# Kernel optimization log

Measured on AMD Instinct MI355X. Metric: run time of the kernel, lower is better.

## Reference

```python
import jax, jax.numpy as jnp
import numpy as np
import math

B, S, D, H = 4, 2048, 512, 8
DK = D // H


def setup_inputs() -> dict:
    key = jax.random.key(0)
    ks = jax.random.split(key, 12)
    def lin(k, scale):
        return jax.random.normal(k, (D, D), dtype=jnp.float32) * scale
    s = 1.0 / math.sqrt(D)
    return {
        "q": jax.random.normal(ks[0], (B, S, D), dtype=jnp.float32),
        "k": jax.random.normal(ks[1], (B, S, D), dtype=jnp.float32),
        "v": jax.random.normal(ks[2], (B, S, D), dtype=jnp.float32),
        "mask": jax.random.randint(ks[3], (B, S, S), 0, 2, dtype=jnp.int32),
        "Wq": lin(ks[4], s), "bq": jnp.zeros((D,), jnp.float32),
        "Wk": lin(ks[5], s), "bk": jnp.zeros((D,), jnp.float32),
        "Wv": lin(ks[6], s), "bv": jnp.zeros((D,), jnp.float32),
        "Wo": lin(ks[7], s), "bo": jnp.zeros((D,), jnp.float32),
    }


def reference(q, k, v, mask, Wq, bq, Wk, bk, Wv, bv, Wo, bo):
    bs = q.shape[0]
    # torch Linear: y = x @ W.T + b
    qh = (q @ Wq.T + bq).reshape(bs, -1, H, DK).transpose(0, 2, 1, 3)  # [b,h,s,dk]
    kh = (k @ Wk.T + bk).reshape(bs, -1, H, DK).transpose(0, 2, 1, 3)
    vh = (v @ Wv.T + bv).reshape(bs, -1, H, DK).transpose(0, 2, 1, 3)
    scores = jnp.einsum("bhqd,bhkd->bhqk", qh, kh) / math.sqrt(DK)
    scores = jnp.where(mask[:, None, :, :] == 0, jnp.float32(-1e9), scores)
    scores = jax.nn.softmax(scores, axis=-1)
    # dropout p=0.0 -> identity
    concat = jnp.einsum("bhqk,bhkd->bhqd", scores, vh)
    concat = concat.transpose(0, 2, 1, 3).reshape(bs, -1, D)
    output = concat @ Wo.T + bo
    return (output, scores)
```

## Files before the change

### kernel.cpp

```cpp
#include <hip/hip_runtime.h>
#include <hip/hip_bf16.h>

#define B_ 4
#define S_ 2048
#define D_ 512
#define H_ 8
#define DK_ 64
#define M_ (B_*S_)

typedef float f32x4 __attribute__((ext_vector_type(4)));
typedef __bf16 bf16x8 __attribute__((ext_vector_type(8)));
typedef unsigned short u16x8 __attribute__((ext_vector_type(8)));

static __device__ __forceinline__ unsigned short f2bf(float x) {
    return __builtin_bit_cast(unsigned short, __float2bfloat16(x));
}
static __device__ __forceinline__ float bf2f(unsigned short u) {
    return __bfloat162float(__builtin_bit_cast(__hip_bfloat16, u));
}
static __device__ __forceinline__ bf16x8 ldfrag(const unsigned short* p) {
    return __builtin_bit_cast(bf16x8, *(const u16x8*)p);
}

static __device__ __forceinline__ void bar_lds() {
    asm volatile("s_waitcnt lgkmcnt(0)\n\ts_barrier" ::: "memory");
}

typedef __attribute__((address_space(1))) const unsigned int gu32;
typedef __attribute__((address_space(3))) unsigned int lu32;
static __device__ __forceinline__ void gl_lds16(const unsigned short* g, unsigned short* l) {
    __builtin_amdgcn_global_load_lds((gu32*)g, (lu32*)l, 16, 0, 0);
}

static __device__ __forceinline__ void split8(const float4 x0, const float4 x1,
                                              u16x8& h, u16x8& l) {
    float f[8] = {x0.x, x0.y, x0.z, x0.w, x1.x, x1.y, x1.z, x1.w};
    #pragma unroll
    for (int j = 0; j < 8; ++j) {
        const unsigned u = __builtin_bit_cast(unsigned, f[j]);
        h[j] = (unsigned short)(u >> 16);
        const float hf = __builtin_bit_cast(float, u & 0xFFFF0000u);
        l[j] = (unsigned short)(__builtin_bit_cast(unsigned, f[j] - hf) >> 16);
    }
}

__global__ __launch_bounds__(256) void split_x3(
    const float* __restrict__ xq, const float* __restrict__ xk, const float* __restrict__ xv,
    unsigned short* __restrict__ qh, unsigned short* __restrict__ qlo,
    unsigned short* __restrict__ kh, unsigned short* __restrict__ klo,
    unsigned short* __restrict__ vh, unsigned short* __restrict__ vlo)
{
    const size_t t = (size_t)blockIdx.x * 256 + threadIdx.x;
    const int z = blockIdx.y;
    const float* in = z == 0 ? xq : z == 1 ? xk : xv;
    unsigned short* oh = z == 0 ? qh : z == 1 ? kh : vh;
    unsigned short* ol = z == 0 ? qlo : z == 1 ? klo : vlo;
    const float4* p = (const float4*)(in + t * 8);
    u16x8 hh, ll;
    split8(p[0], p[1], hh, ll);
    ((u16x8*)oh)[t] = hh;
    ((u16x8*)ol)[t] = ll;
}

__global__ __launch_bounds__(256) void split_w4(
    const float* __restrict__ Wq, const float* __restrict__ Wk,
    const float* __restrict__ Wv, const float* __restrict__ Wo,
    unsigned short* __restrict__ Wcat_h, unsigned short* __restrict__ Wcat_l,
    unsigned short* __restrict__ Wo_h, unsigned short* __restrict__ Wo_l)
{
    const size_t t = (size_t)blockIdx.x * 256 + threadIdx.x;
    const int z = blockIdx.y;
    const float* in = z == 0 ? Wq : z == 1 ? Wk : z == 2 ? Wv : Wo;
    unsigned short* oh = z < 3 ? Wcat_h + (size_t)z * 262144 : Wo_h;
    unsigned short* ol = z < 3 ? Wcat_l + (size_t)z * 262144 : Wo_l;
    const float4* p = (const float4*)(in + t * 8);
    u16x8 hh, ll;
    split8(p[0], p[1], hh, ll);
    ((u16x8*)oh)[t] = hh;
    ((u16x8*)ol)[t] = ll;
}

__global__ __launch_bounds__(256) void mask_pack(
    const int* __restrict__ mask, unsigned long long* __restrict__ bits)
{
    const size_t t = (size_t)blockIdx.x * 256 + threadIdx.x;
    const int m = mask[t];
    const unsigned long long w = __ballot(m != 0);
    if ((threadIdx.x & 63) == 0) bits[t >> 6] = w;
}

#define GBK 32
__global__ __launch_bounds__(256, 2) void gemm_hl(
    const unsigned short* __restrict__ qXh, const unsigned short* __restrict__ qXl,
    const unsigned short* __restrict__ kXh, const unsigned short* __restrict__ kXl,
    const unsigned short* __restrict__ vXh, const unsigned short* __restrict__ vXl,
    const unsigned short* __restrict__ Wh, const unsigned short* __restrict__ Wl,
    const float* __restrict__ b0, const float* __restrict__ b1, const float* __restrict__ b2,
    float* __restrict__ Yf32,
    unsigned short* __restrict__ q_hi, unsigned short* __restrict__ q_lo,
    unsigned short* __restrict__ k_hi, unsigned short* __restrict__ k_lo,
    unsigned short* __restrict__ v_hi, int fused)
{
    __shared__ __align__(16) unsigned short lds[2][4][128 * GBK];

    const int tid = threadIdx.x;
    const int lane = tid & 63, wv = tid >> 6;
    const int quad = lane >> 4, col = lane & 15;
    const int wm = wv >> 1, wn = wv & 1;
    const int m0 = blockIdx.x * 128;
    const int n0g = blockIdx.y * 128;
    const int mat = fused ? (n0g >> 9) : 0;
    const unsigned short* Xh = (!fused || mat == 0) ? qXh : (mat == 1 ? kXh : vXh);
    const unsigned short* Xl = (!fused || mat == 0) ? qXl : (mat == 1 ? kXl : vXl);

    const int rsub = lane >> 2;
    const int csw = (((lane & 3) ^ ((lane >> 3) & 3))) * 8;

    f32x4 acc[4][4] = {};

    auto STAGE = [&](int t, int buf) {
        const int kt = t * GBK;
        #pragma unroll
        for (int i = 0; i < 2; ++i) {
            const int r0 = wv * 32 + i * 16;
            gl_lds16(Xh + (size_t)(m0 + r0 + rsub) * D_ + kt + csw, &lds[buf][0][r0 * GBK]);
            gl_lds16(Xl + (size_t)(m0 + r0 + rsub) * D_ + kt + csw, &lds[buf][1][r0 * GBK]);
            gl_lds16(Wh + (size_t)(n0g + r0 + rsub) * D_ + kt + csw, &lds[buf][2][r0 * GBK]);
            gl_lds16(Wl + (size_t)(n0g + r0 + rsub) * D_ + kt + csw, &lds[buf][3][r0 * GBK]);
        }
    };

    auto COMPUTE = [&](int buf) {
        bf16x8 ah[4], al[4], bh[4], bl[4];
        #pragma unroll
        for (int i = 0; i < 4; ++i) {
            const int ra = wm * 64 + i * 16 + col;
            const int ca = (quad ^ ((ra >> 1) & 3)) * 8;
            ah[i] = ldfrag(&lds[buf][0][ra * GBK + ca]);
            al[i] = ldfrag(&lds[buf][1][ra * GBK + ca]);
            const int rb = wn * 64 + i * 16 + col;
            const int cb = (quad ^ ((rb >> 1) & 3)) * 8;
            bh[i] = ldfrag(&lds[buf][2][rb * GBK + cb]);
            bl[i] = ldfrag(&lds[buf][3][rb * GBK + cb]);
        }
        __builtin_amdgcn_s_setprio(1);
        #pragma unroll
        for (int i = 0; i < 4; ++i)
            #pragma unroll
            for (int j = 0; j < 4; ++j) {
                acc[i][j] = __builtin_amdgcn_mfma_f32_16x16x32_bf16(ah[i], bh[j], acc[i][j], 0, 0, 0);
                acc[i][j] = __builtin_amdgcn_mfma_f32_16x16x32_bf16(al[i], bh[j], acc[i][j], 0, 0, 0);
                acc[i][j] = __builtin_amdgcn_mfma_f32_16x16x32_bf16(ah[i], bl[j], acc[i][j], 0, 0, 0);
            }
        __builtin_amdgcn_s_setprio(0);
    };

    STAGE(0, 0);
    STAGE(1, 1);
    int cur = 0;
    for (int t = 0; t < 16; ++t) {
        if (t < 15) asm volatile("s_waitcnt vmcnt(8)\n\ts_barrier" ::: "memory");
        else        asm volatile("s_waitcnt vmcnt(0)\n\ts_barrier" ::: "memory");
        COMPUTE(cur);
        asm volatile("s_barrier" ::: "memory");
        if (t < 14) STAGE(t + 2, cur);
        cur ^= 1;
    }

    #pragma unroll
    for (int j = 0; j < 4; ++j) {
        const int ng = n0g + wn * 64 + j * 16 + col;
        const int n = fused ? (ng & 511) : ng;
        const float bias = fused ? (mat == 0 ? b0[n] : mat == 1 ? b1[n] : b2[n]) : b0[n];
        #pragma unroll
        for (int i = 0; i < 4; ++i) {
            #pragma unroll
            for (int r = 0; r < 4; ++r) {
                const int m = m0 + wm * 64 + i * 16 + quad * 4 + r;
                const float vv = acc[i][j][r] + bias;
                if (!fused) {
                    Yf32[(size_t)m * D_ + n] = vv;
                } else {
                    const int bi = m >> 11, si = m & (S_ - 1);
                    const int hh = n >> 6, dk = n & 63;
                    const size_t idx = (((size_t)bi * H_ + hh) * S_ + si) * DK_ + dk;
                    const unsigned short hi = f2bf(vv);
                    if (mat == 0)      { q_hi[idx] = hi; q_lo[idx] = f2bf(vv - bf2f(hi)); }
                    else if (mat == 1) { k_hi[idx] = hi; k_lo[idx] = f2bf(vv - bf2f(hi)); }
                    else               { v_hi[idx] = hi; }
                }
            }
        }
    }
}

__global__ __launch_bounds__(256) void attn_mfma_kernel(
    const unsigned short* __restrict__ q_hi, const unsigned short* __restrict__ q_lo,
    const unsigned short* __restrict__ k_hi, const unsigned short* __restrict__ k_lo,
    const unsigned short* __restrict__ v_hi, const unsigned long long* __restrict__ mbits,
    float* __restrict__ scores,
    unsigned short* __restrict__ ch, unsigned short* __restrict__ cl)
{
    __shared__ __align__(16) unsigned short sK2[2][64][72];
    __shared__ __align__(16) unsigned short sVt[64][72];
    __shared__ __align__(16) unsigned short sP[64][72];

    const int tid = threadIdx.x;
    const int q0 = blockIdx.x * 64;
    const int h = blockIdx.y, b = blockIdx.z;
    const size_t bh = (size_t)b * H_ + h;
    const int wv = tid >> 6, lane = tid & 63, quad = lane >> 4, col = lane & 15;
    const int sr = tid >> 2, sc = (tid & 3) * 16;

    float* sPF = (float*)&sK2[0][0][0];

    bf16x8 qh[2], ql[2];
    {
        const size_t qb = (bh * S_ + q0 + wv * 16 + col) * DK_;
        qh[0] = ldfrag(q_hi + qb + quad * 8);
        qh[1] = ldfrag(q_hi + qb + 32 + quad * 8);
        ql[0] = ldfrag(q_lo + qb + quad * 8);
        ql[1] = ldfrag(q_lo + qb + 32 + quad * 8);
    }

    const size_t mrow_base = ((size_t)b * S_ + q0 + wv * 16 + quad * 4) * (S_ / 64);

    u16x8 rkh[2], rkl[2], rv[2];
    auto ld_k = [&](int kt) {
        const u16x8* gh = (const u16x8*)(k_hi + (bh * S_ + kt * 64 + sr) * DK_ + sc);
        const u16x8* gl = (const u16x8*)(k_lo + (bh * S_ + kt * 64 + sr) * DK_ + sc);
        rkh[0] = gh[0]; rkh[1] = gh[1]; rkl[0] = gl[0]; rkl[1] = gl[1];
    };
    auto ld_v = [&](int kt) {
        const u16x8* gv = (const u16x8*)(v_hi + (bh * S_ + kt * 64 + sr) * DK_ + sc);
        rv[0] = gv[0]; rv[1] = gv[1];
    };

    auto compute_svals = [&](const unsigned long long* mw, float sv[4][4]) {
        #pragma unroll
        for (int t = 0; t < 4; ++t) {
            f32x4 acc = {0.f, 0.f, 0.f, 0.f};
            __builtin_amdgcn_s_setprio(1);
            #pragma unroll
            for (int kci = 0; kci < 2; ++kci) {
                bf16x8 bhf = ldfrag(&sK2[0][t * 16 + col][kci * 32 + quad * 8]);
                bf16x8 blf = ldfrag(&sK2[1][t * 16 + col][kci * 32 + quad * 8]);
                acc = __builtin_amdgcn_mfma_f32_16x16x32_bf16(qh[kci], bhf, acc, 0, 0, 0);
                acc = __builtin_amdgcn_mfma_f32_16x16x32_bf16(qh[kci], blf, acc, 0, 0, 0);
                acc = __builtin_amdgcn_mfma_f32_16x16x32_bf16(ql[kci], bhf, acc, 0, 0, 0);
            }
            __builtin_amdgcn_s_setprio(0);
            #pragma unroll
            for (int r = 0; r < 4; ++r) {
                float s = acc[r] * 0.125f;
                if (!((mw[r] >> (t * 16 + col)) & 1ull)) s = -1e9f;
                sv[t][r] = s;
            }
        }
    };

    float m_run[4], l_run[4];
    #pragma unroll
    for (int r = 0; r < 4; ++r) { m_run[r] = -1e30f; l_run[r] = 0.f; }

    ld_k(0);
    for (int kt = 0; kt < 32; ++kt) {
        bar_lds();
        *(u16x8*)&sK2[0][sr][sc] = rkh[0]; *(u16x8*)&sK2[0][sr][sc + 8] = rkh[1];
        *(u16x8*)&sK2[1][sr][sc] = rkl[0]; *(u16x8*)&sK2[1][sr][sc + 8] = rkl[1];
        bar_lds();
        if (kt < 31) ld_k(kt + 1);
        unsigned long long mw[4];
        #pragma unroll
        for (int r = 0; r < 4; ++r) mw[r] = mbits[mrow_base + (size_t)r * (S_ / 64) + kt];
        float sv[4][4];
        compute_svals(mw, sv);
        #pragma unroll
        for (int r = 0; r < 4; ++r) {
            float tm = fmaxf(fmaxf(sv[0][r], sv[1][r]), fmaxf(sv[2][r], sv[3][r]));
            #pragma unroll
            for (int mm = 1; mm < 16; mm <<= 1) tm = fmaxf(tm, __shfl_xor(tm, mm));
            const float nm = fmaxf(m_run[r], tm);
            float ts = __expf(sv[0][r] - nm) + __expf(sv[1][r] - nm)
                     + __expf(sv[2][r] - nm) + __expf(sv[3][r] - nm);
            #pragma unroll
            for (int mm = 1; mm < 16; mm <<= 1) ts += __shfl_xor(ts, mm);
            l_run[r] = l_run[r] * __expf(m_run[r] - nm) + ts;
            m_run[r] = nm;
        }
    }
    float inv_l[4];
    #pragma unroll
    for (int r = 0; r < 4; ++r) inv_l[r] = 1.f / l_run[r];

    f32x4 oacc[4] = {};
    ld_k(0); ld_v(0);
    for (int kt = 0; kt < 32; ++kt) {
        bar_lds();
        *(u16x8*)&sK2[0][sr][sc] = rkh[0]; *(u16x8*)&sK2[0][sr][sc + 8] = rkh[1];
        *(u16x8*)&sK2[1][sr][sc] = rkl[0]; *(u16x8*)&sK2[1][sr][sc + 8] = rkl[1];
        #pragma unroll
        for (int i = 0; i < 8; ++i) { sVt[sc + i][sr] = rv[0][i]; sVt[sc + 8 + i][sr] = rv[1][i]; }
        bar_lds();
        if (kt < 31) { ld_k(kt + 1); ld_v(kt + 1); }
        unsigned long long mw[4];
        #pragma unroll
        for (int r = 0; r < 4; ++r) mw[r] = mbits[mrow_base + (size_t)r * (S_ / 64) + kt];
        float sv[4][4];
        compute_svals(mw, sv);
        float pv[4][4];
        #pragma unroll
        for (int t = 0; t < 4; ++t) {
            #pragma unroll
            for (int r = 0; r < 4; ++r) {
                const float p = __expf(sv[t][r] - m_run[r]) * inv_l[r];
                pv[t][r] = p;
                sP[wv * 16 + quad * 4 + r][t * 16 + col] = f2bf(p);
            }
        }
        bar_lds();
        #pragma unroll
        for (int t = 0; t < 4; ++t)
            #pragma unroll
            for (int r = 0; r < 4; ++r)
                sPF[(wv * 16 + quad * 4 + r) * 68 + t * 16 + col] = pv[t][r];
        #pragma unroll
        for (int rg = 0; rg < 2; ++rg)
            #pragma unroll
            for (int hf = 0; hf < 2; ++hf) {
                const int rl = wv * 16 + rg * 8 + (lane >> 3);
                const int cf = hf * 32 + (lane & 7) * 4;
                const f32x4 pw = *(const f32x4*)&sPF[rl * 68 + cf];
                __builtin_nontemporal_store(pw,
                    (f32x4*)&scores[(bh * S_ + q0 + rl) * S_ + kt * 64 + cf]);
            }
        __builtin_amdgcn_s_setprio(1);
        #pragma unroll
        for (int to = 0; to < 4; ++to) {
            #pragma unroll
            for (int kc = 0; kc < 64; kc += 32) {
                bf16x8 a  = ldfrag(&sP[wv * 16 + col][kc + quad * 8]);
                bf16x8 bb = ldfrag(&sVt[to * 16 + col][kc + quad * 8]);
                oacc[to] = __builtin_amdgcn_mfma_f32_16x16x32_bf16(a, bb, oacc[to], 0, 0, 0);
            }
        }
        __builtin_amdgcn_s_setprio(0);
    }

    #pragma unroll
    for (int to = 0; to < 4; ++to) {
        #pragma unroll
        for (int r = 0; r < 4; ++r) {
            const int qg = q0 + wv * 16 + quad * 4 + r;
            const size_t idx = ((size_t)b * S_ + qg) * D_ + h * DK_ + to * 16 + col;
            const float o = oacc[to][r];
            const unsigned short oh16 = f2bf(o);
            ch[idx] = oh16;
            cl[idx] = f2bf(o - bf2f(oh16));
        }
    }
}

extern "C" void kernel_launch(void* const* d_in, const int* in_sizes, int n_in,
                              void* d_out, int out_size, void* d_ws, size_t ws_size,
                              hipStream_t stream) {
    const float* q  = (const float*)d_in[0];
    const float* k  = (const float*)d_in[1];
    const float* v  = (const float*)d_in[2];
    const int* mask = (const int*)d_in[3];
    const float* Wq = (const float*)d_in[4];  const float* bq = (const float*)d_in[5];
    const float* Wk = (const float*)d_in[6];  const float* bk = (const float*)d_in[7];
    const float* Wv = (const float*)d_in[8];  const float* bv = (const float*)d_in[9];
    const float* Wo = (const float*)d_in[10]; const float* bo = (const float*)d_in[11];

    float* out    = (float*)d_out;
    float* scores = out + (size_t)B_ * S_ * D_;

    const size_t NH = (size_t)B_ * H_ * S_ * DK_;
    unsigned short* W = (unsigned short*)d_ws;
    unsigned short* q_hi = W + 0 * NH;
    unsigned short* q_lo = W + 1 * NH;
    unsigned short* k_hi = W + 2 * NH;
    unsigned short* k_lo = W + 3 * NH;
    unsigned short* v_hi = W + 4 * NH;
    unsigned short* qXh = W + 7 * NH;  unsigned short* qXl = W + 8 * NH;
    unsigned short* kXh = W + 9 * NH;  unsigned short* kXl = W + 10 * NH;
    unsigned short* vXh = W + 11 * NH; unsigned short* vXl = W + 12 * NH;
    unsigned short* cat_h = qXh;       unsigned short* cat_l = qXl;
    unsigned short* Wcat_h = W + 13 * NH;
    unsigned short* Wcat_l = Wcat_h + 786432;
    unsigned short* Wo_h   = Wcat_l + 786432;
    unsigned short* Wo_l   = Wo_h + 262144;
    unsigned long long* mbits = (unsigned long long*)(Wo_l + 262144);

    split_x3<<<dim3(2048, 3), 256, 0, stream>>>(q, k, v, qXh, qXl, kXh, kXl, vXh, vXl);
    split_w4<<<dim3(128, 4), 256, 0, stream>>>(Wq, Wk, Wv, Wo, Wcat_h, Wcat_l, Wo_h, Wo_l);
    mask_pack<<<dim3(65536), 256, 0, stream>>>(mask, mbits);

    gemm_hl<<<dim3(64, 12), 256, 0, stream>>>(
        qXh, qXl, kXh, kXl, vXh, vXl, Wcat_h, Wcat_l, bq, bk, bv,
        nullptr, q_hi, q_lo, k_hi, k_lo, v_hi, 1);

    attn_mfma_kernel<<<dim3(S_ / 64, H_, B_), 256, 0, stream>>>(
        q_hi, q_lo, k_hi, k_lo, v_hi, mbits, scores, cat_h, cat_l);

    gemm_hl<<<dim3(64, 4), 256, 0, stream>>>(
        cat_h, cat_l, nullptr, nullptr, nullptr, nullptr, Wo_h, Wo_l, bo, nullptr, nullptr,
        out, nullptr, nullptr, nullptr, nullptr, nullptr, 0);
}
```

Measured before the change: 917.3 us.

## Load K and V fragments directly from global memory, store V transposed

The attention kernel no longer stages K and V tiles through LDS with barriers. Instead each wave loads its MFMA fragments straight from global memory, and V is written pre-transposed by the projection GEMM so the fragments are contiguous. The probability tile also moves to its own LDS array, which drops a barrier. This removes LDS staging and synchronisation, but every wave now re-reads K/V from global or L2 with no register prefetch, and the transposed V store from the GEMM is strided. There is also no barrier between writing sP/sPF and the cross-lane reads, which relies on per-wave row ownership.

```diff
diff --git a/kernel.cpp b/kernel.cpp
--- a/kernel.cpp
+++ b/kernel.cpp
@@ -20,10 +20,6 @@
 }
 static __device__ __forceinline__ bf16x8 ldfrag(const unsigned short* p) {
     return __builtin_bit_cast(bf16x8, *(const u16x8*)p);
-}
-
-static __device__ __forceinline__ void bar_lds() {
-    asm volatile("s_waitcnt lgkmcnt(0)\n\ts_barrier" ::: "memory");
 }
 
 typedef __attribute__((address_space(1))) const unsigned int gu32;
@@ -99,7 +95,7 @@
     float* __restrict__ Yf32,
     unsigned short* __restrict__ q_hi, unsigned short* __restrict__ q_lo,
     unsigned short* __restrict__ k_hi, unsigned short* __restrict__ k_lo,
-    unsigned short* __restrict__ v_hi, int fused)
+    unsigned short* __restrict__ vT, int fused)
 {
     __shared__ __align__(16) unsigned short lds[2][4][128 * GBK];
 
@@ -183,11 +179,15 @@
                 } else {
                     const int bi = m >> 11, si = m & (S_ - 1);
                     const int hh = n >> 6, dk = n & 63;
-                    const size_t idx = (((size_t)bi * H_ + hh) * S_ + si) * DK_ + dk;
                     const unsigned short hi = f2bf(vv);
-                    if (mat == 0)      { q_hi[idx] = hi; q_lo[idx] = f2bf(vv - bf2f(hi)); }
-                    else if (mat == 1) { k_hi[idx] = hi; k_lo[idx] = f2bf(vv - bf2f(hi)); }
-                    else               { v_hi[idx] = hi; }
+                    if (mat == 2) {
+                        const size_t idxT = (((size_t)bi * H_ + hh) * DK_ + dk) * S_ + si;
+                        vT[idxT] = hi;
+                    } else {
+                        const size_t idx = (((size_t)bi * H_ + hh) * S_ + si) * DK_ + dk;
+                        if (mat == 0) { q_hi[idx] = hi; q_lo[idx] = f2bf(vv - bf2f(hi)); }
+                        else          { k_hi[idx] = hi; k_lo[idx] = f2bf(vv - bf2f(hi)); }
+                    }
                 }
             }
         }
@@ -197,22 +197,18 @@
 __global__ __launch_bounds__(256) void attn_mfma_kernel(
     const unsigned short* __restrict__ q_hi, const unsigned short* __restrict__ q_lo,
     const unsigned short* __restrict__ k_hi, const unsigned short* __restrict__ k_lo,
-    const unsigned short* __restrict__ v_hi, const unsigned long long* __restrict__ mbits,
+    const unsigned short* __restrict__ vT, const unsigned long long* __restrict__ mbits,
     float* __restrict__ scores,
     unsigned short* __restrict__ ch, unsigned short* __restrict__ cl)
 {
-    __shared__ __align__(16) unsigned short sK2[2][64][72];
-    __shared__ __align__(16) unsigned short sVt[64][72];
     __shared__ __align__(16) unsigned short sP[64][72];
+    __shared__ __align__(16) float sPF[64][68];
 
     const int tid = threadIdx.x;
     const int q0 = blockIdx.x * 64;
     const int h = blockIdx.y, b = blockIdx.z;
     const size_t bh = (size_t)b * H_ + h;
     const int wv = tid >> 6, lane = tid & 63, quad = lane >> 4, col = lane & 15;
-    const int sr = tid >> 2, sc = (tid & 3) * 16;
-
-    float* sPF = (float*)&sK2[0][0][0];
 
     bf16x8 qh[2], ql[2];
     {
@@ -224,32 +220,25 @@
     }
 
     const size_t mrow_base = ((size_t)b * S_ + q0 + wv * 16 + quad * 4) * (S_ / 64);
-
-    u16x8 rkh[2], rkl[2], rv[2];
-    auto ld_k = [&](int kt) {
-        const u16x8* gh = (const u16x8*)(k_hi + (bh * S_ + kt * 64 + sr) * DK_ + sc);
-        const u16x8* gl = (const u16x8*)(k_lo + (bh * S_ + kt * 64 + sr) * DK_ + sc);
-        rkh[0] = gh[0]; rkh[1] = gh[1]; rkl[0] = gl[0]; rkl[1] = gl[1];
-    };
-    auto ld_v = [&](int kt) {
-        const u16x8* gv = (const u16x8*)(v_hi + (bh * S_ + kt * 64 + sr) * DK_ + sc);
-        rv[0] = gv[0]; rv[1] = gv[1];
-    };
-
-    auto compute_svals = [&](const unsigned long long* mw, float sv[4][4]) {
+    const unsigned short* kH = k_hi + bh * S_ * DK_;
+    const unsigned short* kL = k_lo + bh * S_ * DK_;
+    const unsigned short* vB = vT + bh * DK_ * S_;
+
+    auto compute_svals = [&](int kt, const unsigned long long* mw, float sv[4][4]) {
         #pragma unroll
         for (int t = 0; t < 4; ++t) {
+            const size_t krow = (size_t)(kt * 64 + t * 16 + col) * DK_;
             f32x4 acc = {0.f, 0.f, 0.f, 0.f};
-            __builtin_amdgcn_s_setprio(1);
             #pragma unroll
             for (int kci = 0; kci < 2; ++kci) {
-                bf16x8 bhf = ldfrag(&sK2[0][t * 16 + col][kci * 32 + quad * 8]);
-                bf16x8 blf = ldfrag(&sK2[1][t * 16 + col][kci * 32 + quad * 8]);
+                bf16x8 bhf = ldfrag(kH + krow + kci * 32 + quad * 8);
+                bf16x8 blf = ldfrag(kL + krow + kci * 32 + quad * 8);
+                __builtin_amdgcn_s_setprio(1);
                 acc = __builtin_amdgcn_mfma_f32_16x16x32_bf16(qh[kci], bhf, acc, 0, 0, 0);
                 acc = __builtin_amdgcn_mfma_f32_16x16x32_bf16(qh[kci], blf, acc, 0, 0, 0);
                 acc = __builtin_amdgcn_mfma_f32_16x16x32_bf16(ql[kci], bhf, acc, 0, 0, 0);
-            }
-            __builtin_amdgcn_s_setprio(0);
+                __builtin_amdgcn_s_setprio(0);
+            }
             #pragma unroll
             for (int r = 0; r < 4; ++r) {
                 float s = acc[r] * 0.125f;
@@ -263,18 +252,12 @@
     #pragma unroll
     for (int r = 0; r < 4; ++r) { m_run[r] = -1e30f; l_run[r] = 0.f; }
 
-    ld_k(0);
     for (int kt = 0; kt < 32; ++kt) {
-        bar_lds();
-        *(u16x8*)&sK2[0][sr][sc] = rkh[0]; *(u16x8*)&sK2[0][sr][sc + 8] = rkh[1];
-        *(u16x8*)&sK2[1][sr][sc] = rkl[0]; *(u16x8*)&sK2[1][sr][sc + 8] = rkl[1];
-        bar_lds();
-        if (kt < 31) ld_k(kt + 1);
         unsigned long long mw[4];
         #pragma unroll
         for (int r = 0; r < 4; ++r) mw[r] = mbits[mrow_base + (size_t)r * (S_ / 64) + kt];
         float sv[4][4];
-        compute_svals(mw, sv);
+        compute_svals(kt, mw, sv);
         #pragma unroll
         for (int r = 0; r < 4; ++r) {
             float tm = fmaxf(fmaxf(sv[0][r], sv[1][r]), fmaxf(sv[2][r], sv[3][r]));
@@ -294,57 +277,43 @@
     for (int r = 0; r < 4; ++r) inv_l[r] = 1.f / l_run[r];
 
     f32x4 oacc[4] = {};
-    ld_k(0); ld_v(0);
     for (int kt = 0; kt < 32; ++kt) {
-        bar_lds();
-        *(u16x8*)&sK2[0][sr][sc] = rkh[0]; *(u16x8*)&sK2[0][sr][sc + 8] = rkh[1];
-        *(u16x8*)&sK2[1][sr][sc] = rkl[0]; *(u16x8*)&sK2[1][sr][sc + 8] = rkl[1];
-        #pragma unroll
-        for (int i = 0; i < 8; ++i) { sVt[sc + i][sr] = rv[0][i]; sVt[sc + 8 + i][sr] = rv[1][i]; }
-        bar_lds();
-        if (kt < 31) { ld_k(kt + 1); ld_v(kt + 1); }
         unsigned long long mw[4];
         #pragma unroll
         for (int r = 0; r < 4; ++r) mw[r] = mbits[mrow_base + (size_t)r * (S_ / 64) + kt];
         float sv[4][4];
-        compute_svals(mw, sv);
-        float pv[4][4];
+        compute_svals(kt, mw, sv);
         #pragma unroll
         for (int t = 0; t < 4; ++t) {
             #pragma unroll
             for (int r = 0; r < 4; ++r) {
                 const float p = __expf(sv[t][r] - m_run[r]) * inv_l[r];
-                pv[t][r] = p;
+                sPF[wv * 16 + quad * 4 + r][t * 16 + col] = p;
                 sP[wv * 16 + quad * 4 + r][t * 16 + col] = f2bf(p);
             }
         }
-        bar_lds();
-        #pragma unroll
-        for (int t = 0; t < 4; ++t)
-            #pragma unroll
-            for (int r = 0; r < 4; ++r)
-                sPF[(wv * 16 + quad * 4 + r) * 68 + t * 16 + col] = pv[t][r];
         #pragma unroll
         for (int rg = 0; rg < 2; ++rg)
             #pragma unroll
             for (int hf = 0; hf < 2; ++hf) {
                 const int rl = wv * 16 + rg * 8 + (lane >> 3);
                 const int cf = hf * 32 + (lane & 7) * 4;
-                const f32x4 pw = *(const f32x4*)&sPF[rl * 68 + cf];
+                const f32x4 pw = *(const f32x4*)&sPF[rl][cf];
                 __builtin_nontemporal_store(pw,
                     (f32x4*)&scores[(bh * S_ + q0 + rl) * S_ + kt * 64 + cf]);
             }
-        __builtin_amdgcn_s_setprio(1);
         #pragma unroll
         for (int to = 0; to < 4; ++to) {
+            const size_t vrow = (size_t)(to * 16 + col) * S_ + kt * 64;
             #pragma unroll
             for (int kc = 0; kc < 64; kc += 32) {
                 bf16x8 a  = ldfrag(&sP[wv * 16 + col][kc + quad * 8]);
-                bf16x8 bb = ldfrag(&sVt[to * 16 + col][kc + quad * 8]);
+                bf16x8 bb = ldfrag(vB + vrow + kc + quad * 8);
+                __builtin_amdgcn_s_setprio(1);
                 oacc[to] = __builtin_amdgcn_mfma_f32_16x16x32_bf16(a, bb, oacc[to], 0, 0, 0);
-            }
-        }
-        __builtin_amdgcn_s_setprio(0);
+                __builtin_amdgcn_s_setprio(0);
+            }
+        }
     }
 
     #pragma unroll
@@ -382,7 +351,7 @@
     unsigned short* q_lo = W + 1 * NH;
     unsigned short* k_hi = W + 2 * NH;
     unsigned short* k_lo = W + 3 * NH;
-    unsigned short* v_hi = W + 4 * NH;
+    unsigned short* vT   = W + 4 * NH;
     unsigned short* qXh = W + 7 * NH;  unsigned short* qXl = W + 8 * NH;
     unsigned short* kXh = W + 9 * NH;  unsigned short* kXl = W + 10 * NH;
     unsigned short* vXh = W + 11 * NH; unsigned short* vXl = W + 12 * NH;
@@ -399,10 +368,10 @@
 
     gemm_hl<<<dim3(64, 12), 256, 0, stream>>>(
         qXh, qXl, kXh, kXl, vXh, vXl, Wcat_h, Wcat_l, bq, bk, bv,
-        nullptr, q_hi, q_lo, k_hi, k_lo, v_hi, 1);
+        nullptr, q_hi, q_lo, k_hi, k_lo, vT, 1);
 
     attn_mfma_kernel<<<dim3(S_ / 64, H_, B_), 256, 0, stream>>>(
-        q_hi, q_lo, k_hi, k_lo, v_hi, mbits, scores, cat_h, cat_l);
+        q_hi, q_lo, k_hi, k_lo, vT, mbits, scores, cat_h, cat_l);
 
     gemm_hl<<<dim3(64, 4), 256, 0, stream>>>(
         cat_h, cat_l, nullptr, nullptr, nullptr, nullptr, Wo_h, Wo_l, bo, nullptr, nullptr,
```

Measured after the change: 1.240 ms. +35.2%, slower.
